# Optimization experiments

Measured on AMD Instinct MI355X. Metric: run time of the kernel, lower is better.

Reference implementation:

```python
import jax, jax.numpy as jnp
import numpy as np

B, S, D = 1, 2048, 2048
H, G, HD = 32, 8, 64          # heads, kv groups, head_dim
GS = H // G                   # group size = 4
EPS = 1e-6


def _rmsnorm(v, w):
    vf = v.astype(jnp.float32)
    n = vf * jax.lax.rsqrt(jnp.mean(vf * vf, axis=-1, keepdims=True) + EPS)
    return (n * (1.0 + w.astype(jnp.float32))).astype(v.dtype)


def _rope(v, cos, sin):
    # v: [b, h, s, hd]; cos/sin: [s, hd] (rot_dim == head_dim)
    half = v.shape[-1] // 2
    x1, x2 = v[..., :half], v[..., half:]
    rotated = jnp.concatenate([-x2, x1], axis=-1)
    c = cos[None, None, :, :]
    s = sin[None, None, :, :]
    return (v * c + rotated * s).astype(v.dtype)


def setup_inputs() -> dict:
    key = jax.random.key(0)
    ks = jax.random.split(key, 8)
    x = jax.random.normal(ks[0], (B, S, D), dtype=jnp.float32)
    # causal mask: True above diagonal => masked out
    mask = jnp.triu(jnp.ones((S, S), dtype=bool), k=1)
    # standard RoPE tables, full rotary dim == head_dim
    inv_freq = 1.0 / (10000.0 ** (jnp.arange(0, HD, 2, dtype=jnp.float32) / HD))
    angles = jnp.arange(S, dtype=jnp.float32)[:, None] * inv_freq[None, :]
    angles = jnp.concatenate([angles, angles], axis=-1)  # [S, HD]
    cos = jnp.cos(angles)
    sin = jnp.sin(angles)
    sc = 1.0 / np.sqrt(D)
    Wq = jax.random.normal(ks[1], (2 * H * HD, D), dtype=jnp.float32) * sc
    Wk = jax.random.normal(ks[2], (G * HD, D), dtype=jnp.float32) * sc
    Wv = jax.random.normal(ks[3], (G * HD, D), dtype=jnp.float32) * sc
    Wo = jax.random.normal(ks[4], (D, H * HD), dtype=jnp.float32) * sc
    q_norm_w = jnp.zeros((HD,), dtype=jnp.float32)
    k_norm_w = jnp.zeros((HD,), dtype=jnp.float32)
    return {"x": x, "mask": mask, "cos": cos, "sin": sin, "Wq": Wq,
            "Wk": Wk, "Wv": Wv, "Wo": Wo,
            "q_norm_w": q_norm_w, "k_norm_w": k_norm_w}


def reference(x, mask, cos, sin, Wq, Wk, Wv, Wo, q_norm_w, k_norm_w):
    b, s, _ = x.shape
    d_out = H * HD
    # fused q + gate projection: [b, s, H, 2*HD]
    qg = jnp.einsum('bsd,ed->bse', x, Wq).reshape(b, s, H, 2 * HD)
    q = qg[..., :HD]                         # [b, s, H, HD]
    gate = qg[..., HD:].reshape(b, s, d_out)  # [b, s, d_out]
    k = jnp.einsum('bsd,ed->bse', x, Wk).reshape(b, s, G, HD)
    v = jnp.einsum('bsd,ed->bse', x, Wv).reshape(b, s, G, HD)
    q = q.transpose(0, 2, 1, 3)   # [b, H, s, HD]
    k = k.transpose(0, 2, 1, 3)   # [b, G, s, HD]
    v = v.transpose(0, 2, 1, 3)
    q = _rmsnorm(q, q_norm_w)
    k = _rmsnorm(k, k_norm_w)
    q = _rope(q, cos[:s], sin[:s])
    k = _rope(k, cos[:s], sin[:s])
    # GQA without materializing repeated K/V: group queries as [b, G, GS, s, HD]
    qg_ = q.reshape(b, G, GS, s, HD)
    scores = jnp.einsum('bghqd,bgkd->bghqk', qg_, k)   # [b, G, GS, s, s]
    scores = jnp.where(mask[None, None, None, :s, :s], -jnp.inf, scores)
    scale = HD ** (-0.5)
    w = jax.nn.softmax((scores * scale).astype(jnp.float32), axis=-1).astype(q.dtype)
    ctx = jnp.einsum('bghqk,bgkd->bghqd', w, v)        # [b, G, GS, s, HD]
    ctx = ctx.reshape(b, H, s, HD).transpose(0, 2, 1, 3).reshape(b, s, d_out)
    ctx = ctx * jax.nn.sigmoid(gate)
    return jnp.einsum('bse,de->bsd', ctx, Wo)
```

## Files before the change

### kernel.cpp

```cpp
#include <hip/hip_runtime.h>

typedef __bf16 bf16;
typedef __bf16 bf16x4 __attribute__((ext_vector_type(4)));
typedef __bf16 bf16x8 __attribute__((ext_vector_type(8)));
typedef float f32x4 __attribute__((ext_vector_type(4)));

#define DEV static __device__ __forceinline__

constexpr int S  = 2048;
constexpr int D  = 2048;
constexpr int H  = 32;
constexpr int G  = 8;
constexpr int HD = 64;
constexpr int NQG = 2 * H * HD;
constexpr int NKV = G * HD;
constexpr int LDP = 72;

DEV bf16x8 load8(const bf16* p) { return *reinterpret_cast<const bf16x8*>(p); }

DEV f32x4 mfma16(bf16x8 a, bf16x8 b, f32x4 c) {
  return __builtin_amdgcn_mfma_f32_16x16x32_bf16(a, b, c, 0, 0, 0);
}

DEV void gload_lds16(const bf16* g, bf16* l) {
  __builtin_amdgcn_global_load_lds(
      (const __attribute__((address_space(1))) void*)g,
      (__attribute__((address_space(3))) void*)l, 16, 0, 0);
}

template <int NISS>
DEV void stage_tile(bf16* lds, const bf16* src_row0, size_t ld, int k0, int tid) {
  const int w = tid >> 6, l = tid & 63;
#pragma unroll
  for (int i = 0; i < NISS; ++i) {
    int blk = w * NISS + i;
    int r = blk * 8 + (l >> 3);
    int c = (l & 7) ^ (r & 7);
    gload_lds16(src_row0 + (size_t)r * ld + k0 + c * 8, lds + blk * 512);
  }
}

DEV void stage64_8w(bf16* lds, const bf16* src_row0, size_t ld, int k0, int tid) {
  const int w = tid >> 6, l = tid & 63;
  int r = w * 8 + (l >> 3);
  int c = (l & 7) ^ (r & 7);
  gload_lds16(src_row0 + (size_t)r * ld + k0 + c * 8, lds + w * 512);
}

DEV bf16x8 fragr(const bf16* T, int row, int chunk) {
  return load8(T + row * 64 + (((chunk ^ (row & 7)) << 3)));
}

DEV float fexp2(float x) { return __builtin_amdgcn_exp2f(x); }
DEV float frcp(float x)  { return __builtin_amdgcn_rcpf(x); }

__global__ __launch_bounds__(256) void cvt_all(
    const float* __restrict__ x,  const float* __restrict__ wq,
    const float* __restrict__ wk, const float* __restrict__ wv,
    const float* __restrict__ wo,
    bf16* __restrict__ xb,  bf16* __restrict__ wqb, bf16* __restrict__ wkb,
    bf16* __restrict__ wvb, bf16* __restrict__ wob)
{
  long c = (long)blockIdx.x * 256 + threadIdx.x;
  const float* src; bf16* dst; long off;
  if      (c <  524288) { src = x;  dst = xb;  off = c; }
  else if (c < 1572864) { src = wq; dst = wqb; off = c -  524288; }
  else if (c < 1703936) { src = wk; dst = wkb; off = c - 1572864; }
  else if (c < 1835008) { src = wv; dst = wvb; off = c - 1703936; }
  else                  { src = wo; dst = wob; off = c - 1835008; }
  long i = off * 8;
  const float4* p = reinterpret_cast<const float4*>(src + i);
  float4 a = p[0], b = p[1];
  bf16x8 o;
  o[0] = (bf16)a.x; o[1] = (bf16)a.y; o[2] = (bf16)a.z; o[3] = (bf16)a.w;
  o[4] = (bf16)b.x; o[5] = (bf16)b.y; o[6] = (bf16)b.z; o[7] = (bf16)b.w;
  *reinterpret_cast<bf16x8*>(dst + i) = o;
}

__global__ __launch_bounds__(256, 3) void gemm_qkv(
    const bf16* __restrict__ X, const bf16* __restrict__ Wq,
    const bf16* __restrict__ Wk, const bf16* __restrict__ Wv,
    bf16* __restrict__ qg, bf16* __restrict__ kpre, bf16* __restrict__ vt)
{
  __shared__ __align__(16) bf16 As[128 * 64];
  __shared__ __align__(16) bf16 Bs[128 * 64];

  const int tid  = threadIdx.x;
  const int wave = tid >> 6;
  const int lane = tid & 63;
  const int ln = lane & 15, hi = lane >> 4;
  const int wm = wave >> 1, wn = wave & 1;
  const int m0 = blockIdx.y * 128;
  const int nt = blockIdx.x;

  const bf16* W; int n0;
  if (nt < 32)      { W = Wq; n0 = nt * 128; }
  else if (nt < 36) { W = Wk; n0 = (nt - 32) * 128; }
  else              { W = Wv; n0 = (nt - 36) * 128; }

  const bf16* arow = X + (size_t)m0 * D;
  const bf16* brow = W + (size_t)n0 * D;

  f32x4 acc[4][4] = {};

  for (int k0 = 0; k0 < D; k0 += 64) {
    __syncthreads();
    stage_tile<4>(As, arow, D, k0, tid);
    stage_tile<4>(Bs, brow, D, k0, tid);
    __syncthreads();
#pragma unroll
    for (int kk = 0; kk < 64; kk += 32) {
      bf16x8 a[4], b[4];
#pragma unroll
      for (int mi = 0; mi < 4; ++mi) a[mi] = fragr(As, wm * 64 + mi * 16 + ln, (kk >> 3) + hi);
#pragma unroll
      for (int ni = 0; ni < 4; ++ni) b[ni] = fragr(Bs, wn * 64 + ni * 16 + ln, (kk >> 3) + hi);
#pragma unroll
      for (int mi = 0; mi < 4; ++mi)
#pragma unroll
        for (int ni = 0; ni < 4; ++ni)
          acc[mi][ni] = mfma16(a[mi], b[ni], acc[mi][ni]);
    }
  }

  if (nt < 36) {
    bf16* C; int ldc;
    if (nt < 32) { C = qg; ldc = NQG; } else { C = kpre; ldc = NKV; }
#pragma unroll
    for (int mi = 0; mi < 4; ++mi)
#pragma unroll
      for (int ni = 0; ni < 4; ++ni)
#pragma unroll
        for (int j = 0; j < 4; ++j) {
          int r = m0 + wm * 64 + mi * 16 + hi * 4 + j;
          int c = n0 + wn * 64 + ni * 16 + ln;
          C[(size_t)r * ldc + c] = (bf16)acc[mi][ni][j];
        }
  } else {
    int nrel = (nt - 36) * 128;
#pragma unroll
    for (int mi = 0; mi < 4; ++mi)
#pragma unroll
      for (int ni = 0; ni < 4; ++ni)
#pragma unroll
        for (int j = 0; j < 4; ++j) {
          int r = m0 + wm * 64 + mi * 16 + hi * 4 + j;
          int c = nrel + wn * 64 + ni * 16 + ln;
          vt[(size_t)c * S + r] = (bf16)acc[mi][ni][j];
        }
  }
}

__global__ __launch_bounds__(256, 3) void gemm_out(
    const bf16* __restrict__ A, const bf16* __restrict__ W,
    float* __restrict__ C)
{
  __shared__ __align__(16) bf16 As[128 * 64];
  __shared__ __align__(16) bf16 Bs[64 * 64];

  const int tid  = threadIdx.x;
  const int wave = tid >> 6;
  const int lane = tid & 63;
  const int ln = lane & 15, hi = lane >> 4;
  const int m0 = blockIdx.y * 128;
  const int n0 = blockIdx.x * 64;

  const bf16* arow = A + (size_t)m0 * D;
  const bf16* brow = W + (size_t)n0 * D;

  f32x4 acc[2][4] = {};

  for (int k0 = 0; k0 < D; k0 += 64) {
    __syncthreads();
    stage_tile<4>(As, arow, D, k0, tid);
    stage_tile<2>(Bs, brow, D, k0, tid);
    __syncthreads();
#pragma unroll
    for (int kk = 0; kk < 64; kk += 32) {
      bf16x8 a[2], b[4];
#pragma unroll
      for (int mi = 0; mi < 2; ++mi) a[mi] = fragr(As, wave * 32 + mi * 16 + ln, (kk >> 3) + hi);
#pragma unroll
      for (int ni = 0; ni < 4; ++ni) b[ni] = fragr(Bs, ni * 16 + ln, (kk >> 3) + hi);
#pragma unroll
      for (int mi = 0; mi < 2; ++mi)
#pragma unroll
        for (int ni = 0; ni < 4; ++ni)
          acc[mi][ni] = mfma16(a[mi], b[ni], acc[mi][ni]);
    }
  }

#pragma unroll
  for (int mi = 0; mi < 2; ++mi)
#pragma unroll
    for (int ni = 0; ni < 4; ++ni)
#pragma unroll
      for (int j = 0; j < 4; ++j) {
        int r = m0 + wave * 32 + mi * 16 + hi * 4 + j;
        int c = n0 + ni * 16 + ln;
        C[(size_t)r * D + c] = acc[mi][ni][j];
      }
}

__global__ __launch_bounds__(256) void rmsrope(
    const bf16* __restrict__ qg, const bf16* __restrict__ kpre,
    const float* __restrict__ cosb, const float* __restrict__ sinb,
    const float* __restrict__ qw, const float* __restrict__ kw,
    bf16* __restrict__ qrot, bf16* __restrict__ krot)
{
  int wid  = (int)((blockIdx.x * (unsigned)blockDim.x + threadIdx.x) >> 6);
  int lane = threadIdx.x & 63;
  int s  = wid & (S - 1);
  int hh = wid >> 11;

  float v, wgt;
  if (hh < H) { v = (float)qg[(size_t)s * NQG + hh * 128 + lane];        wgt = qw[lane]; }
  else        { v = (float)kpre[(size_t)s * NKV + (hh - H) * 64 + lane]; wgt = kw[lane]; }

  float ss = v * v;
#pragma unroll
  for (int m = 1; m < 64; m <<= 1) ss += __shfl_xor(ss, m);
  float xf = v * (1.0f / sqrtf(ss * (1.0f / 64.0f) + 1e-6f)) * (1.0f + wgt);

  float part = __shfl_xor(xf, 32);
  float rot  = (lane < 32) ? -part : part;
  float c  = cosb[(size_t)s * HD + lane];
  float sn = sinb[(size_t)s * HD + lane];
  float r  = xf * c + rot * sn;

  if (hh < H) {
    qrot[((size_t)hh * S + s) * HD + lane] = (bf16)(r * 0.18033688011111204f);
  } else {
    krot[((size_t)(hh - H) * S + s) * HD + lane] = (bf16)r;
  }
}

#define BARRIER() asm volatile("s_barrier" ::: "memory")
#define VMDRAIN() asm volatile("s_waitcnt vmcnt(0)" ::: "memory")

DEV void attn_phase(const bf16* __restrict__ qrot, const bf16* __restrict__ krow,
                    const bf16* __restrict__ vrow, const bf16* __restrict__ qg,
                    bf16* __restrict__ ctxg,
                    bf16* Kb0, bf16* Kb1, bf16* Vb0, bf16* Vb1, bf16* pw,
                    int h, int qchunk, int nt, int ln, int hi, int tid)
{
  const int qb = qchunk * 64 + ((tid >> 6) & 3) * 16;
  const int q  = qb + ln;

  const bf16* qbase = qrot + ((size_t)h * S + qb + ln) * HD + hi * 8;
  bf16x8 q0 = load8(qbase);
  bf16x8 q1 = load8(qbase + 32);

  f32x4 po[4] = {};
  float m = -INFINITY, l = 0.f;

  stage64_8w(Kb0, krow, 64, 0, tid);
  stage64_8w(Vb0, vrow, S, 0, tid);
  VMDRAIN();
  BARRIER();

  int cur = 0;
  for (int t = 0; t < nt; ++t) {
    const bf16* Kb = cur ? Kb1 : Kb0;
    const bf16* Vb = cur ? Vb1 : Vb0;

    if (t + 1 < nt) {
      bf16* Kn = cur ? Kb0 : Kb1;
      bf16* Vn = cur ? Vb0 : Vb1;
      stage64_8w(Kn, krow + (size_t)(t + 1) * 64 * 64, 64, 0, tid);
      stage64_8w(Vn, vrow, S, (t + 1) * 64, tid);
    }

    bf16x8 kf0[4], kf1[4];
#pragma unroll
    for (int kr = 0; kr < 4; ++kr) {
      kf0[kr] = fragr(Kb, kr * 16 + ln, hi);
      kf1[kr] = fragr(Kb, kr * 16 + ln, hi + 4);
    }
    bf16x8 bv0[4], bv1[4];
#pragma unroll
    for (int dt = 0; dt < 4; ++dt) {
      bv0[dt] = fragr(Vb, dt * 16 + ln, hi);
      bv1[dt] = fragr(Vb, dt * 16 + ln, hi + 4);
    }

    f32x4 sc[4] = {};
    __builtin_amdgcn_s_setprio(1);
#pragma unroll
    for (int kr = 0; kr < 4; ++kr) {
      sc[kr] = mfma16(kf0[kr], q0, sc[kr]);
      sc[kr] = mfma16(kf1[kr], q1, sc[kr]);
    }
    __builtin_amdgcn_s_setprio(0);

    float pmax = -INFINITY;
    if (t == nt - 1) {
      const int key0 = t << 6;
#pragma unroll
      for (int kr = 0; kr < 4; ++kr)
#pragma unroll
        for (int j = 0; j < 4; ++j) {
          int key = key0 + kr * 16 + hi * 4 + j;
          float v = (key <= q) ? sc[kr][j] : -INFINITY;
          sc[kr][j] = v;
          pmax = fmaxf(pmax, v);
        }
    } else {
#pragma unroll
      for (int kr = 0; kr < 4; ++kr)
#pragma unroll
        for (int j = 0; j < 4; ++j) pmax = fmaxf(pmax, sc[kr][j]);
    }
    pmax = fmaxf(pmax, __shfl_xor(pmax, 16));
    pmax = fmaxf(pmax, __shfl_xor(pmax, 32));

    if (__any(pmax > m + 8.0f)) {
      float mn = fmaxf(m, pmax);
      float c  = fexp2(m - mn);
      l *= c;
      float cc[4];
#pragma unroll
      for (int j = 0; j < 4; ++j) cc[j] = __shfl(c, hi * 4 + j);
#pragma unroll
      for (int dt = 0; dt < 4; ++dt)
#pragma unroll
        for (int j = 0; j < 4; ++j) po[dt][j] *= cc[j];
      m = mn;
    }

    float ps = 0.f;
#pragma unroll
    for (int kr = 0; kr < 4; ++kr)
#pragma unroll
      for (int j = 0; j < 4; ++j) {
        float e = fexp2(sc[kr][j] - m);
        sc[kr][j] = e;
        ps += e;
      }
    ps += __shfl_xor(ps, 16);
    ps += __shfl_xor(ps, 32);
    l += ps;

#pragma unroll
    for (int kr = 0; kr < 4; ++kr) {
      unsigned w0, w1;
      asm("v_cvt_pk_bf16_f32 %0, %1, %2" : "=v"(w0) : "v"(sc[kr][0]), "v"(sc[kr][1]));
      asm("v_cvt_pk_bf16_f32 %0, %1, %2" : "=v"(w1) : "v"(sc[kr][2]), "v"(sc[kr][3]));
      uint2 w = {w0, w1};
      *reinterpret_cast<uint2*>(pw + ln * LDP + kr * 16 + hi * 4) = w;
    }
    bf16x8 pa0 = load8(pw + ln * LDP + hi * 8);
    bf16x8 pa1 = load8(pw + ln * LDP + 32 + hi * 8);

    __builtin_amdgcn_s_setprio(1);
#pragma unroll
    for (int dt = 0; dt < 4; ++dt) {
      po[dt] = mfma16(pa0, bv0[dt], po[dt]);
      po[dt] = mfma16(pa1, bv1[dt], po[dt]);
    }
    __builtin_amdgcn_s_setprio(0);

    VMDRAIN();
    BARRIER();
    cur ^= 1;
  }

  float lf[4];
#pragma unroll
  for (int j = 0; j < 4; ++j) lf[j] = __shfl(l, hi * 4 + j);
#pragma unroll
  for (int dt = 0; dt < 4; ++dt)
#pragma unroll
    for (int j = 0; j < 4; ++j) {
      int qq = qb + hi * 4 + j;
      int d  = dt * 16 + ln;
      float o  = po[dt][j] * frcp(lf[j]);
      float gv = (float)qg[(size_t)qq * NQG + h * 128 + 64 + d];
      float sg = frcp(1.0f + fexp2(gv * -1.442695040888963f));
      ctxg[(size_t)qq * D + h * 64 + d] = (bf16)(o * sg);
    }
}

__global__ __launch_bounds__(512) void attn(
    const bf16* __restrict__ qrot, const bf16* __restrict__ krot,
    const bf16* __restrict__ vt, const bf16* __restrict__ qg,
    bf16* __restrict__ ctxg)
{
  __shared__ __align__(16) bf16 Kbuf[2][64 * 64];
  __shared__ __align__(16) bf16 Vbuf[2][64 * 64];
  __shared__ __align__(16) bf16 Pl[8][16 * LDP];

  const int tid  = threadIdx.x;
  const int lane = tid & 63;
  const int ln = lane & 15, hi = lane >> 4;

  const int bid = blockIdx.x;
  const int g   = bid & 7;
  const int i   = bid >> 3;
  const int hp  = i & 1;
  const int pr  = i >> 1;
  const int h   = g * 4 + hp * 2 + ((tid >> 6) >> 2);
  bf16* pw = &Pl[tid >> 6][0];

  const bf16* krow = krot + (size_t)g * S * HD;
  const bf16* vrow = vt + (size_t)g * 64 * S;

  attn_phase(qrot, krow, vrow, qg, ctxg,
             &Kbuf[0][0], &Kbuf[1][0], &Vbuf[0][0], &Vbuf[1][0], pw,
             h, pr, pr + 1, ln, hi, tid);
  attn_phase(qrot, krow, vrow, qg, ctxg,
             &Kbuf[0][0], &Kbuf[1][0], &Vbuf[0][0], &Vbuf[1][0], pw,
             h, 31 - pr, 32 - pr, ln, hi, tid);
}

extern "C" void kernel_launch(void* const* d_in, const int* in_sizes, int n_in,
                              void* d_out, int out_size, void* d_ws, size_t ws_size,
                              hipStream_t stream) {
  const float* x    = (const float*)d_in[0];
  const float* cosb = (const float*)d_in[2];
  const float* sinb = (const float*)d_in[3];
  const float* Wq   = (const float*)d_in[4];
  const float* Wk   = (const float*)d_in[5];
  const float* Wv   = (const float*)d_in[6];
  const float* Wo   = (const float*)d_in[7];
  const float* qw   = (const float*)d_in[8];
  const float* kw   = (const float*)d_in[9];

  char* ws = (char*)d_ws;
  bf16* xb   = (bf16*)(ws);
  bf16* Wqb  = (bf16*)(ws + ( 8u << 20));
  bf16* Wkb  = (bf16*)(ws + (24u << 20));
  bf16* Wvb  = (bf16*)(ws + (26u << 20));
  bf16* Wob  = (bf16*)(ws + (28u << 20));
  bf16* qg   = (bf16*)(ws + (36u << 20));
  bf16* kpre = (bf16*)(ws + (52u << 20));
  bf16* vt   = (bf16*)(ws + (54u << 20));
  bf16* qrot = (bf16*)(ws + (56u << 20));
  bf16* krot = (bf16*)(ws + (64u << 20));
  bf16* ctxg = (bf16*)(ws + (66u << 20));
  float* out = (float*)d_out;

  cvt_all<<<dim3(9216), 256, 0, stream>>>(x, Wq, Wk, Wv, Wo,
                                          xb, Wqb, Wkb, Wvb, Wob);

  gemm_qkv<<<dim3(40, 16), 256, 0, stream>>>(xb, Wqb, Wkb, Wvb, qg, kpre, vt);
  rmsrope<<<dim3(20480), 256, 0, stream>>>(qg, kpre, cosb, sinb, qw, kw, qrot, krot);
  attn<<<dim3(256), 512, 0, stream>>>(qrot, krot, vt, qg, ctxg);
  gemm_out<<<dim3(32, 16), 256, 0, stream>>>(ctxg, Wob, out);
}
```

Measured before the change: 146.1 us.

## Fuse RMSNorm+RoPE into QKV GEMM epilogue and enlarge output GEMM tiles

Moves q/k RMSNorm and rotary embedding into the QKV GEMM epilogue, reducing across the 16-lane groups that share a head row, and writes rotated q/k directly. This removes the separate rmsrope launch and the write and re-read of the pre-norm q/k tensors. Separately, the output projection GEMM grows from a 128x64 to a 128x128 tile with a 2x2 wave layout, halving the block count and improving operand reuse. The epilogue now does scattered cos/sin loads, and the larger output tile cuts parallelism to 256 blocks.

```diff
diff --git a/kernel.cpp b/kernel.cpp
--- a/kernel.cpp
+++ b/kernel.cpp
@@ -13,7 +13,6 @@
 constexpr int G  = 8;
 constexpr int HD = 64;
 constexpr int NQG = 2 * H * HD;
-constexpr int NKV = G * HD;
 constexpr int LDP = 72;
 
 DEV bf16x8 load8(const bf16* p) { return *reinterpret_cast<const bf16x8*>(p); }
@@ -77,10 +76,48 @@
   *reinterpret_cast<bf16x8*>(dst + i) = o;
 }
 
+DEV void rms_rope_store(f32x4 acc[4][4], bf16* __restrict__ dst,
+                        const float* __restrict__ w,
+                        const float* __restrict__ cosb,
+                        const float* __restrict__ sinb,
+                        int s0, int ln, int hi, float outscale)
+{
+  float wgt[4];
+#pragma unroll
+  for (int ni = 0; ni < 4; ++ni) wgt[ni] = 1.0f + w[ni * 16 + ln];
+#pragma unroll
+  for (int mi = 0; mi < 4; ++mi)
+#pragma unroll
+    for (int j = 0; j < 4; ++j) {
+      int s = s0 + mi * 16 + hi * 4 + j;
+      float v0 = acc[mi][0][j], v1 = acc[mi][1][j];
+      float v2 = acc[mi][2][j], v3 = acc[mi][3][j];
+      float ss = v0 * v0 + v1 * v1 + v2 * v2 + v3 * v3;
+      ss += __shfl_xor(ss, 1);
+      ss += __shfl_xor(ss, 2);
+      ss += __shfl_xor(ss, 4);
+      ss += __shfl_xor(ss, 8);
+      float inv = __builtin_amdgcn_rsqf(ss * (1.0f / 64.0f) + 1e-6f);
+      float xf[4] = {v0 * inv * wgt[0], v1 * inv * wgt[1],
+                     v2 * inv * wgt[2], v3 * inv * wgt[3]};
+#pragma unroll
+      for (int ni = 0; ni < 4; ++ni) {
+        int d = ni * 16 + ln;
+        float c  = cosb[s * HD + d];
+        float sn = sinb[s * HD + d];
+        float rot = (ni < 2) ? -xf[ni + 2] : xf[ni - 2];
+        dst[(size_t)s * HD + d] = (bf16)((xf[ni] * c + rot * sn) * outscale);
+      }
+    }
+}
+
 __global__ __launch_bounds__(256, 3) void gemm_qkv(
     const bf16* __restrict__ X, const bf16* __restrict__ Wq,
     const bf16* __restrict__ Wk, const bf16* __restrict__ Wv,
-    bf16* __restrict__ qg, bf16* __restrict__ kpre, bf16* __restrict__ vt)
+    const float* __restrict__ cosb, const float* __restrict__ sinb,
+    const float* __restrict__ qw, const float* __restrict__ kw,
+    bf16* __restrict__ qg, bf16* __restrict__ qrot,
+    bf16* __restrict__ krot, bf16* __restrict__ vt)
 {
   __shared__ __align__(16) bf16 As[128 * 64];
   __shared__ __align__(16) bf16 Bs[128 * 64];
@@ -123,19 +160,27 @@
     }
   }
 
-  if (nt < 36) {
-    bf16* C; int ldc;
-    if (nt < 32) { C = qg; ldc = NQG; } else { C = kpre; ldc = NKV; }
-#pragma unroll
-    for (int mi = 0; mi < 4; ++mi)
-#pragma unroll
-      for (int ni = 0; ni < 4; ++ni)
-#pragma unroll
-        for (int j = 0; j < 4; ++j) {
-          int r = m0 + wm * 64 + mi * 16 + hi * 4 + j;
-          int c = n0 + wn * 64 + ni * 16 + ln;
-          C[(size_t)r * ldc + c] = (bf16)acc[mi][ni][j];
-        }
+  const int s0 = m0 + wm * 64;
+  if (nt < 32) {
+    if (wn == 0) {
+      rms_rope_store(acc, qrot + (size_t)nt * S * HD, qw, cosb, sinb,
+                     s0, ln, hi, 0.18033688011111204f);
+    } else {
+#pragma unroll
+      for (int mi = 0; mi < 4; ++mi)
+#pragma unroll
+        for (int ni = 0; ni < 4; ++ni)
+#pragma unroll
+          for (int j = 0; j < 4; ++j) {
+            int r = s0 + mi * 16 + hi * 4 + j;
+            int c = nt * 128 + 64 + ni * 16 + ln;
+            qg[(size_t)r * NQG + c] = (bf16)acc[mi][ni][j];
+          }
+    }
+  } else if (nt < 36) {
+    int g8 = (nt - 32) * 2 + wn;
+    rms_rope_store(acc, krot + (size_t)g8 * S * HD, kw, cosb, sinb,
+                   s0, ln, hi, 1.0f);
   } else {
     int nrel = (nt - 36) * 128;
 #pragma unroll
@@ -144,7 +189,7 @@
       for (int ni = 0; ni < 4; ++ni)
 #pragma unroll
         for (int j = 0; j < 4; ++j) {
-          int r = m0 + wm * 64 + mi * 16 + hi * 4 + j;
+          int r = s0 + mi * 16 + hi * 4 + j;
           int c = nrel + wn * 64 + ni * 16 + ln;
           vt[(size_t)c * S + r] = (bf16)acc[mi][ni][j];
         }
@@ -156,34 +201,35 @@
     float* __restrict__ C)
 {
   __shared__ __align__(16) bf16 As[128 * 64];
-  __shared__ __align__(16) bf16 Bs[64 * 64];
+  __shared__ __align__(16) bf16 Bs[128 * 64];
 
   const int tid  = threadIdx.x;
   const int wave = tid >> 6;
   const int lane = tid & 63;
   const int ln = lane & 15, hi = lane >> 4;
+  const int wm = wave >> 1, wn = wave & 1;
   const int m0 = blockIdx.y * 128;
-  const int n0 = blockIdx.x * 64;
+  const int n0 = blockIdx.x * 128;
 
   const bf16* arow = A + (size_t)m0 * D;
   const bf16* brow = W + (size_t)n0 * D;
 
-  f32x4 acc[2][4] = {};
+  f32x4 acc[4][4] = {};
 
   for (int k0 = 0; k0 < D; k0 += 64) {
     __syncthreads();
     stage_tile<4>(As, arow, D, k0, tid);
-    stage_tile<2>(Bs, brow, D, k0, tid);
+    stage_tile<4>(Bs, brow, D, k0, tid);
     __syncthreads();
 #pragma unroll
     for (int kk = 0; kk < 64; kk += 32) {
-      bf16x8 a[2], b[4];
-#pragma unroll
-      for (int mi = 0; mi < 2; ++mi) a[mi] = fragr(As, wave * 32 + mi * 16 + ln, (kk >> 3) + hi);
-#pragma unroll
-      for (int ni = 0; ni < 4; ++ni) b[ni] = fragr(Bs, ni * 16 + ln, (kk >> 3) + hi);
-#pragma unroll
-      for (int mi = 0; mi < 2; ++mi)
+      bf16x8 a[4], b[4];
+#pragma unroll
+      for (int mi = 0; mi < 4; ++mi) a[mi] = fragr(As, wm * 64 + mi * 16 + ln, (kk >> 3) + hi);
+#pragma unroll
+      for (int ni = 0; ni < 4; ++ni) b[ni] = fragr(Bs, wn * 64 + ni * 16 + ln, (kk >> 3) + hi);
+#pragma unroll
+      for (int mi = 0; mi < 4; ++mi)
 #pragma unroll
         for (int ni = 0; ni < 4; ++ni)
           acc[mi][ni] = mfma16(a[mi], b[ni], acc[mi][ni]);
@@ -191,48 +237,15 @@
   }
 
 #pragma unroll
-  for (int mi = 0; mi < 2; ++mi)
+  for (int mi = 0; mi < 4; ++mi)
 #pragma unroll
     for (int ni = 0; ni < 4; ++ni)
 #pragma unroll
       for (int j = 0; j < 4; ++j) {
-        int r = m0 + wave * 32 + mi * 16 + hi * 4 + j;
-        int c = n0 + ni * 16 + ln;
+        int r = m0 + wm * 64 + mi * 16 + hi * 4 + j;
+        int c = n0 + wn * 64 + ni * 16 + ln;
         C[(size_t)r * D + c] = acc[mi][ni][j];
       }
-}
-
-__global__ __launch_bounds__(256) void rmsrope(
-    const bf16* __restrict__ qg, const bf16* __restrict__ kpre,
-    const float* __restrict__ cosb, const float* __restrict__ sinb,
-    const float* __restrict__ qw, const float* __restrict__ kw,
-    bf16* __restrict__ qrot, bf16* __restrict__ krot)
-{
-  int wid  = (int)((blockIdx.x * (unsigned)blockDim.x + threadIdx.x) >> 6);
-  int lane = threadIdx.x & 63;
-  int s  = wid & (S - 1);
-  int hh = wid >> 11;
-
-  float v, wgt;
-  if (hh < H) { v = (float)qg[(size_t)s * NQG + hh * 128 + lane];        wgt = qw[lane]; }
-  else        { v = (float)kpre[(size_t)s * NKV + (hh - H) * 64 + lane]; wgt = kw[lane]; }
-
-  float ss = v * v;
-#pragma unroll
-  for (int m = 1; m < 64; m <<= 1) ss += __shfl_xor(ss, m);
-  float xf = v * (1.0f / sqrtf(ss * (1.0f / 64.0f) + 1e-6f)) * (1.0f + wgt);
-
-  float part = __shfl_xor(xf, 32);
-  float rot  = (lane < 32) ? -part : part;
-  float c  = cosb[(size_t)s * HD + lane];
-  float sn = sinb[(size_t)s * HD + lane];
-  float r  = xf * c + rot * sn;
-
-  if (hh < H) {
-    qrot[((size_t)hh * S + s) * HD + lane] = (bf16)(r * 0.18033688011111204f);
-  } else {
-    krot[((size_t)(hh - H) * S + s) * HD + lane] = (bf16)r;
-  }
 }
 
 #define BARRIER() asm volatile("s_barrier" ::: "memory")
@@ -433,7 +446,6 @@
   bf16* Wvb  = (bf16*)(ws + (26u << 20));
   bf16* Wob  = (bf16*)(ws + (28u << 20));
   bf16* qg   = (bf16*)(ws + (36u << 20));
-  bf16* kpre = (bf16*)(ws + (52u << 20));
   bf16* vt   = (bf16*)(ws + (54u << 20));
   bf16* qrot = (bf16*)(ws + (56u << 20));
   bf16* krot = (bf16*)(ws + (64u << 20));
@@ -443,8 +455,9 @@
   cvt_all<<<dim3(9216), 256, 0, stream>>>(x, Wq, Wk, Wv, Wo,
                                           xb, Wqb, Wkb, Wvb, Wob);
 
-  gemm_qkv<<<dim3(40, 16), 256, 0, stream>>>(xb, Wqb, Wkb, Wvb, qg, kpre, vt);
-  rmsrope<<<dim3(20480), 256, 0, stream>>>(qg, kpre, cosb, sinb, qw, kw, qrot, krot);
+  gemm_qkv<<<dim3(40, 16), 256, 0, stream>>>(xb, Wqb, Wkb, Wvb,
+                                             cosb, sinb, qw, kw,
+                                             qg, qrot, krot, vt);
   attn<<<dim3(256), 512, 0, stream>>>(qrot, krot, vt, qg, ctxg);
-  gemm_out<<<dim3(32, 16), 256, 0, stream>>>(ctxg, Wob, out);
-}
+  gemm_out<<<dim3(16, 16), 256, 0, stream>>>(ctxg, Wob, out);
+}
```

Result: no change. 145.3 us (-0.5%).
